# Kernel tuning notes

Measured on AMD Instinct MI355X. Metric: run time of the kernel, lower is better.

Reference implementation:

```python
import jax, jax.numpy as jnp
import numpy as np

N = 20000      # nodes
E = 120000     # directed edges (self-loops added in reference, per PyG default)
F_IN = 235
HID = 256
HEADS = 8
NEG_SLOPE = 0.2


def setup_inputs() -> dict:
    key = jax.random.key(0)
    ks = jax.random.split(key, 24)
    p = lambda k, shape: (jax.random.normal(k, shape, jnp.float32) * 0.05)
    inp = {}
    inp["x"] = jax.random.normal(ks[0], (N, F_IN), jnp.float32)
    inp["edge_index"] = jax.random.randint(ks[1], (2, E), 0, N, jnp.int32)
    # input projection
    inp["w_in"] = p(ks[2], (F_IN, HID)); inp["b_in"] = jnp.zeros((HID,), jnp.float32)
    # temporal MLP
    inp["w_t1"] = p(ks[3], (HID, HID)); inp["b_t1"] = jnp.zeros((HID,), jnp.float32)
    inp["w_t2"] = p(ks[4], (HID, HID)); inp["b_t2"] = jnp.zeros((HID,), jnp.float32)
    # GAT layer 1: heads=8, out_per_head=32, concat -> 256
    C1 = HID // HEADS
    inp["w_g1"] = p(ks[5], (HID, HEADS * C1)); inp["a_src1"] = p(ks[6], (HEADS, C1))
    inp["a_dst1"] = p(ks[7], (HEADS, C1)); inp["b_g1"] = jnp.zeros((HEADS * C1,), jnp.float32)
    # GAT layer 2: same shape
    inp["w_g2"] = p(ks[8], (HID, HEADS * C1)); inp["a_src2"] = p(ks[9], (HEADS, C1))
    inp["a_dst2"] = p(ks[10], (HEADS, C1)); inp["b_g2"] = jnp.zeros((HEADS * C1,), jnp.float32)
    # GAT layer 3: heads=8, out_per_head=256, concat -> 2048
    inp["w_g3"] = p(ks[11], (HID, HEADS * HID)); inp["a_src3"] = p(ks[12], (HEADS, HID))
    inp["a_dst3"] = p(ks[13], (HEADS, HID)); inp["b_g3"] = jnp.zeros((HEADS * HID,), jnp.float32)
    # classifier
    inp["w_c1"] = p(ks[14], (2 * HID, HID)); inp["b_c1"] = jnp.zeros((HID,), jnp.float32)
    inp["w_c2"] = p(ks[15], (HID, 2)); inp["b_c2"] = jnp.zeros((2,), jnp.float32)
    return inp


def _gat(x, src, dst, W, a_src, a_dst, b, C):
    """PyG-style GATConv: gather -> per-edge logits -> segment softmax -> scatter-add."""
    h = (x @ W).reshape(-1, HEADS, C)                       # [N, H, C]
    alpha_s = jnp.sum(h * a_src, axis=-1)                   # [N, H]
    alpha_d = jnp.sum(h * a_dst, axis=-1)                   # [N, H]
    e = jax.nn.leaky_relu(alpha_s[src] + alpha_d[dst], NEG_SLOPE)   # [Etot, H]
    m = jax.ops.segment_max(e, dst, num_segments=N)         # [N, H] (self-loops ensure non-empty)
    ex = jnp.exp(e - m[dst])
    den = jax.ops.segment_sum(ex, dst, num_segments=N)
    alpha = ex / (den[dst] + 1e-16)                          # [Etot, H]
    out = jax.ops.segment_sum(alpha[:, :, None] * h[src], dst, num_segments=N)  # [N, H, C]
    return out.reshape(-1, HEADS * C) + b


def reference(x, edge_index, w_in, b_in, w_t1, b_t1, w_t2, b_t2,
              w_g1, a_src1, a_dst1, b_g1, w_g2, a_src2, a_dst2, b_g2,
              w_g3, a_src3, a_dst3, b_g3, w_c1, b_c1, w_c2, b_c2):
    h = jax.nn.elu(x @ w_in + b_in)                          # [N, 256]
    t = jax.nn.relu(h @ w_t1 + b_t1) @ w_t2 + b_t2          # [N, 256] (dropout inactive in eval)
    loop = jnp.arange(N, dtype=edge_index.dtype)
    src = jnp.concatenate([edge_index[0], loop])
    dst = jnp.concatenate([edge_index[1], loop])
    g = jax.nn.elu(_gat(h, src, dst, w_g1, a_src1, a_dst1, b_g1, HID // HEADS))
    g = jax.nn.elu(_gat(g, src, dst, w_g2, a_src2, a_dst2, b_g2, HID // HEADS))
    g = jax.nn.elu(_gat(g, src, dst, w_g3, a_src3, a_dst3, b_g3, HID))  # [N, 2048]
    g = g.reshape(N, HEADS, HID).mean(axis=1)                # [N, 256]
    comb = jnp.concatenate([g, t], axis=-1)                  # [N, 512]
    logits = jax.nn.relu(comb @ w_c1 + b_c1) @ w_c2 + b_c2   # [N, 2]
    return logits
```

## Files before the change

kernel.cpp:

```cpp
#include <hip/hip_runtime.h>
#include <hip/hip_bf16.h>
#include <math.h>


#define HID 256
#define HEADS 8
#define FIN 235

typedef __attribute__((ext_vector_type(8))) short short8;
typedef __attribute__((ext_vector_type(4))) float floatx4;

__device__ __forceinline__ float elu_f(float x) { return x > 0.f ? x : __expf(x) - 1.f; }
__device__ __forceinline__ float bf2f(unsigned short u) {
  return __uint_as_float(((unsigned int)u) << 16);
}
__device__ __forceinline__ unsigned short f2bfu(float f) {
  union { __hip_bfloat16 b; unsigned short u; } c;
  c.b = __float2bfloat16(f);
  return c.u;
}

__global__ void xc_k(const float* __restrict__ x, __hip_bfloat16* __restrict__ xb,
                     const int* __restrict__ ei, int* __restrict__ deg,
                     const float* __restrict__ b2, float* __restrict__ out,
                     int M, int E, int xblocks, int cblocks) {
  int b = blockIdx.x;
  if (b < xblocks) {
    int id = b * 256 + threadIdx.x;
    if (id >= M * 256) return;
    int m = id >> 8, k = id & 255;
    xb[id] = (k < FIN) ? __float2bfloat16(x[(size_t)m * FIN + k]) : __float2bfloat16(0.f);
  } else if (b < xblocks + cblocks) {
    int i = (b - xblocks) * 256 + threadIdx.x;
    if (i < E) atomicAdd(&deg[ei[E + i]], 1);
  } else {
    int i = (b - xblocks - cblocks) * 256 + threadIdx.x;
    if (i < M * 2) out[i] = b2[i & 1];
  }
}

__global__ void wprep_k(const float* __restrict__ w_in, const float* __restrict__ w_t1,
                        const float* __restrict__ w_g1, const float* __restrict__ w_t2,
                        const float* __restrict__ w_g2, const float* __restrict__ w_c1,
                        const float* __restrict__ w_g3, const float* __restrict__ a_s3,
                        const float* __restrict__ a_d3, __hip_bfloat16* __restrict__ wtin,
                        __hip_bfloat16* __restrict__ wtpair, __hip_bfloat16* __restrict__ wtt2,
                        __hip_bfloat16* __restrict__ wtg2, __hip_bfloat16* __restrict__ wtc1,
                        __hip_bfloat16* __restrict__ wtg3s, float* __restrict__ apj) {
  __shared__ float t[32][33];
  int z = blockIdx.z;
  if (z == 14) {
    int idx = (blockIdx.y * 8 + blockIdx.x) * 256 + threadIdx.y * 32 + threadIdx.x;
    if (idx < 256 * 16) {
      int k = idx >> 4, o = idx & 15;
      int h = o >> 1;
      const float* av = (o & 1) ? (a_d3 + h * 256) : (a_s3 + h * 256);
      const float* wr = w_g3 + (size_t)k * 2048 + h * 256;
      float s = 0.f;
      for (int c = 0; c < 256; c++) s += wr[c] * av[c];
      apj[idx] = s;
    }
    return;
  }
  const float* src;
  __hip_bfloat16* dst;
  int K, Kpad, Nstride;
  if (z == 5) {
    src = w_c1; dst = wtc1; K = 512; Kpad = 512; Nstride = 256;
  } else {
    if (blockIdx.y >= 8) return;
    switch (z) {
      case 0: src = w_in; dst = wtin; K = FIN; Kpad = 256; Nstride = 256; break;
      case 1: src = w_t1; dst = wtpair; K = 256; Kpad = 256; Nstride = 256; break;
      case 2: src = w_g1; dst = wtpair + 256 * 256; K = 256; Kpad = 256; Nstride = 256; break;
      case 3: src = w_t2; dst = wtt2; K = 256; Kpad = 256; Nstride = 256; break;
      case 4: src = w_g2; dst = wtg2; K = 256; Kpad = 256; Nstride = 256; break;
      default: {
        int h = z - 6;
        src = w_g3 + h * 256; dst = wtg3s + h * 256; K = 256; Kpad = 2048; Nstride = 2048;
      }
    }
  }
  int nb = blockIdx.x * 32, kb = blockIdx.y * 32;
  int tx = threadIdx.x, ty = threadIdx.y;
#pragma unroll
  for (int j = 0; j < 32; j += 8) {
    int k = kb + ty + j;
    t[ty + j][tx] = (k < K) ? src[(size_t)k * Nstride + nb + tx] : 0.f;
  }
  __syncthreads();
#pragma unroll
  for (int j = 0; j < 32; j += 8) {
    int n = nb + ty + j;
    int k = kb + tx;
    dst[(size_t)n * Kpad + k] = __float2bfloat16(t[tx][ty + j]);
  }
}

__global__ void scan_k(const int* __restrict__ deg, int* __restrict__ rp, int n) {
  __shared__ int wsum[16];
  __shared__ int s_carry;
  int tid = threadIdx.x, lane = tid & 63, wid = tid >> 6;
  if (tid == 0) { s_carry = 0; rp[0] = 0; }
  __syncthreads();
  for (int base = 0; base < n; base += 1024) {
    int i = base + tid;
    int x = (i < n) ? (deg[i] + 1) : 0;
#pragma unroll
    for (int off = 1; off < 64; off <<= 1) {
      int y = __shfl_up(x, off);
      if (lane >= off) x += y;
    }
    if (lane == 63) wsum[wid] = x;
    __syncthreads();
    if (wid == 0 && lane < 16) {
      int s = wsum[lane];
#pragma unroll
      for (int off = 1; off < 16; off <<= 1) {
        int y = __shfl_up(s, off);
        if (lane >= off) s += y;
      }
      wsum[lane] = s;
    }
    __syncthreads();
    int offset = s_carry + (wid > 0 ? wsum[wid - 1] : 0);
    if (i < n) rp[i + 1] = offset + x;
    __syncthreads();
    if (tid == 1023) s_carry += wsum[15];
    __syncthreads();
  }
}

__global__ void fill_k(const int* __restrict__ ei, const int* __restrict__ rp,
                       int* __restrict__ fillc, int* __restrict__ colA, int E, int n) {
  int i = blockIdx.x * blockDim.x + threadIdx.x;
  if (i < E) {
    int d = ei[E + i];
    int pos = rp[d] + atomicAdd(&fillc[d], 1);
    colA[pos] = ei[i];
  } else if (i < E + n) {
    int v = i - E;
    int pos = rp[v] + atomicAdd(&fillc[v], 1);
    colA[pos] = v;
  }
}

template <int ACT, int ALPHA>
__global__ __launch_bounds__(256) void mgemm64_k(
    const __hip_bfloat16* __restrict__ A, const __hip_bfloat16* __restrict__ Bt,
    const float* __restrict__ bias, __hip_bfloat16* __restrict__ Cb,
    int ldc, int M, int N, int K, const float* __restrict__ a_s,
    const float* __restrict__ a_d, float* __restrict__ as_, float* __restrict__ ad_) {
  __shared__ short As[64 * 40];
  __shared__ short Bs[64 * 40];
  int tid = threadIdx.x;
  int row0 = blockIdx.y * 64, col0 = blockIdx.x * 64;
  int w = tid >> 6, lane = tid & 63;
  int wr = w >> 1, wc = w & 1;
  int quad = lane >> 4, l16 = lane & 15;
  floatx4 zero = {0.f, 0.f, 0.f, 0.f};
  floatx4 acc[2][2];
#pragma unroll
  for (int i = 0; i < 2; i++)
#pragma unroll
    for (int j = 0; j < 2; j++) acc[i][j] = zero;

  int srow = tid >> 2, sq = tid & 3;
  const __hip_bfloat16* Ap = A + (size_t)(row0 + srow) * K + sq * 8;
  const __hip_bfloat16* Bp = Bt + (size_t)(col0 + srow) * K + sq * 8;
  bool aok = (row0 + srow) < M;

  uint4 a1 = make_uint4(0, 0, 0, 0);
  if (aok) a1 = *(const uint4*)(Ap);
  uint4 b1 = *(const uint4*)(Bp);

  for (int k0 = 0; k0 < K; k0 += 32) {
    __syncthreads();
    *(uint4*)&As[srow * 40 + sq * 8] = a1;
    *(uint4*)&Bs[srow * 40 + sq * 8] = b1;
    int kn = k0 + 32;
    if (kn < K) {
      if (aok) a1 = *(const uint4*)(Ap + kn);
      b1 = *(const uint4*)(Bp + kn);
    }
    __syncthreads();
    short8 fa[2], fb[2];
#pragma unroll
    for (int i = 0; i < 2; i++) {
      fa[i] = *(const short8*)&As[(wr * 32 + i * 16 + l16) * 40 + quad * 8];
      fb[i] = *(const short8*)&Bs[(wc * 32 + i * 16 + l16) * 40 + quad * 8];
    }
#pragma unroll
    for (int mi = 0; mi < 2; mi++)
#pragma unroll
      for (int ni = 0; ni < 2; ni++)
        acc[mi][ni] = __builtin_amdgcn_mfma_f32_16x16x32_bf16(fa[mi], fb[ni], acc[mi][ni], 0, 0, 0);
  }

#pragma unroll
  for (int mi = 0; mi < 2; mi++) {
    int rbase = row0 + wr * 32 + mi * 16 + quad * 4;
#pragma unroll
    for (int ni = 0; ni < 2; ni++) {
      int c = col0 + wc * 32 + ni * 16 + l16;
      float bv = bias ? bias[c] : 0.f;
#pragma unroll
      for (int reg = 0; reg < 4; reg++) {
        int rr = rbase + reg;
        if (rr >= M) continue;
        float v = acc[mi][ni][reg] + bv;
        if (ACT == 1) v = fmaxf(v, 0.f);
        if (ACT == 2) v = elu_f(v);
        Cb[(size_t)rr * ldc + c] = __float2bfloat16(v);
      }
    }
  }

  if (ALPHA) {
    int h = 2 * blockIdx.x + wc;
    float aS0 = a_s[h * 32 + l16], aS1 = a_s[h * 32 + 16 + l16];
    float aD0 = a_d[h * 32 + l16], aD1 = a_d[h * 32 + 16 + l16];
#pragma unroll
    for (int mi = 0; mi < 2; mi++)
#pragma unroll
      for (int reg = 0; reg < 4; reg++) {
        float pS = acc[mi][0][reg] * aS0 + acc[mi][1][reg] * aS1;
        float pD = acc[mi][0][reg] * aD0 + acc[mi][1][reg] * aD1;
#pragma unroll
        for (int off = 1; off < 16; off <<= 1) {
          pS += __shfl_xor(pS, off);
          pD += __shfl_xor(pD, off);
        }
        if (l16 == 0) {
          int r = row0 + wr * 32 + mi * 16 + quad * 4 + reg;
          if (r < M) {
            as_[r * 8 + h] = pS;
            ad_[r * 8 + h] = pD;
          }
        }
      }
  }
}

__global__ __launch_bounds__(256) void mgemm_dual_k(
    const __hip_bfloat16* __restrict__ A, const __hip_bfloat16* __restrict__ Bt,
    const float* __restrict__ bias1, __hip_bfloat16* __restrict__ O1,
    __hip_bfloat16* __restrict__ O2, int M, const float* __restrict__ a_s1,
    const float* __restrict__ a_d1, float* __restrict__ as_, float* __restrict__ ad_) {
  const int K = 256;
  __shared__ short As[64 * 40];
  __shared__ short Bs[128 * 40];
  int tid = threadIdx.x;
  int row0 = blockIdx.y * 64, col0 = blockIdx.x * 128;
  int w = tid >> 6, lane = tid & 63;
  int wr = w >> 1, wc = w & 1;
  int quad = lane >> 4, l16 = lane & 15;
  floatx4 zero = {0.f, 0.f, 0.f, 0.f};
  floatx4 acc[2][4];
#pragma unroll
  for (int i = 0; i < 2; i++)
#pragma unroll
    for (int j = 0; j < 4; j++) acc[i][j] = zero;

  int srow = tid >> 2, sq = tid & 3;
  const __hip_bfloat16* Ap = A + (size_t)(row0 + srow) * K + sq * 8;
  const __hip_bfloat16* Bp1 = Bt + (size_t)(col0 + srow) * K + sq * 8;
  const __hip_bfloat16* Bp2 = Bt + (size_t)(col0 + 64 + srow) * K + sq * 8;
  bool aok = (row0 + srow) < M;

  uint4 a1 = make_uint4(0, 0, 0, 0);
  if (aok) a1 = *(const uint4*)(Ap);
  uint4 b1 = *(const uint4*)(Bp1);
  uint4 b2 = *(const uint4*)(Bp2);

  for (int k0 = 0; k0 < K; k0 += 32) {
    __syncthreads();
    *(uint4*)&As[srow * 40 + sq * 8] = a1;
    *(uint4*)&Bs[srow * 40 + sq * 8] = b1;
    *(uint4*)&Bs[(64 + srow) * 40 + sq * 8] = b2;
    int kn = k0 + 32;
    if (kn < K) {
      if (aok) a1 = *(const uint4*)(Ap + kn);
      b1 = *(const uint4*)(Bp1 + kn);
      b2 = *(const uint4*)(Bp2 + kn);
    }
    __syncthreads();
    short8 fa[2], fb[4];
#pragma unroll
    for (int i = 0; i < 2; i++)
      fa[i] = *(const short8*)&As[(wr * 32 + i * 16 + l16) * 40 + quad * 8];
#pragma unroll
    for (int i = 0; i < 4; i++)
      fb[i] = *(const short8*)&Bs[(wc * 64 + i * 16 + l16) * 40 + quad * 8];
#pragma unroll
    for (int mi = 0; mi < 2; mi++)
#pragma unroll
      for (int ni = 0; ni < 4; ni++)
        acc[mi][ni] = __builtin_amdgcn_mfma_f32_16x16x32_bf16(fa[mi], fb[ni], acc[mi][ni], 0, 0, 0);
  }

#pragma unroll
  for (int mi = 0; mi < 2; mi++) {
    int rbase = row0 + wr * 32 + mi * 16 + quad * 4;
#pragma unroll
    for (int ni = 0; ni < 4; ni++) {
      int c = col0 + wc * 64 + ni * 16 + l16;
      bool first = c < 256;
      float bv = first ? bias1[c] : 0.f;
      int cc = first ? c : (c - 256);
#pragma unroll
      for (int reg = 0; reg < 4; reg++) {
        int rr = rbase + reg;
        if (rr >= M) continue;
        float v = acc[mi][ni][reg] + bv;
        if (first) v = fmaxf(v, 0.f);
        __hip_bfloat16* dst = first ? O1 : O2;
        dst[(size_t)rr * 256 + cc] = __float2bfloat16(v);
      }
    }
  }

  if (blockIdx.x >= 2) {
    int hb = (blockIdx.x - 2) * 4 + wc * 2;
    float aSA0 = a_s1[hb * 32 + l16], aSA1 = a_s1[hb * 32 + 16 + l16];
    float aDA0 = a_d1[hb * 32 + l16], aDA1 = a_d1[hb * 32 + 16 + l16];
    float aSB0 = a_s1[(hb + 1) * 32 + l16], aSB1 = a_s1[(hb + 1) * 32 + 16 + l16];
    float aDB0 = a_d1[(hb + 1) * 32 + l16], aDB1 = a_d1[(hb + 1) * 32 + 16 + l16];
#pragma unroll
    for (int mi = 0; mi < 2; mi++)
#pragma unroll
      for (int reg = 0; reg < 4; reg++) {
        float pSA = acc[mi][0][reg] * aSA0 + acc[mi][1][reg] * aSA1;
        float pDA = acc[mi][0][reg] * aDA0 + acc[mi][1][reg] * aDA1;
        float pSB = acc[mi][2][reg] * aSB0 + acc[mi][3][reg] * aSB1;
        float pDB = acc[mi][2][reg] * aDB0 + acc[mi][3][reg] * aDB1;
#pragma unroll
        for (int off = 1; off < 16; off <<= 1) {
          pSA += __shfl_xor(pSA, off);
          pDA += __shfl_xor(pDA, off);
          pSB += __shfl_xor(pSB, off);
          pDB += __shfl_xor(pDB, off);
        }
        if (l16 == 0) {
          int r = row0 + wr * 32 + mi * 16 + quad * 4 + reg;
          if (r < M) {
            as_[r * 8 + hb] = pSA;
            ad_[r * 8 + hb] = pDA;
            as_[r * 8 + hb + 1] = pSB;
            ad_[r * 8 + hb + 1] = pDB;
          }
        }
      }
  }
}

__global__ __launch_bounds__(256) void mgemm3_k(
    const __hip_bfloat16* __restrict__ A, const __hip_bfloat16* __restrict__ Bt,
    const float* __restrict__ bias, __hip_bfloat16* __restrict__ comb, int M) {
  const int K = 2048;
  __shared__ short As[64 * 40];
  __shared__ short Bs[64 * 40];
  int tid = threadIdx.x;
  int mg = (M + 63) >> 6;
  int total = mg * 4;
  int F = blockIdx.y * 4 + blockIdx.x;
  int Fmain = (total >> 5) << 5;
  int bx, by;
  if (F < Fmain) {
    by = (F >> 5) * 8 + (F & 7);
    bx = (F >> 3) & 3;
  } else {
    by = ((total >> 5) << 3) + ((F - Fmain) >> 2);
    bx = (F - Fmain) & 3;
  }
  int row0 = by * 64, col0 = bx * 64;
  int w = tid >> 6, lane = tid & 63;
  int wr = w >> 1, wc = w & 1;
  int quad = lane >> 4, l16 = lane & 15;
  floatx4 zero = {0.f, 0.f, 0.f, 0.f};
  floatx4 acc[2][2], sum[2][2];
#pragma unroll
  for (int i = 0; i < 2; i++)
#pragma unroll
    for (int j = 0; j < 2; j++) { acc[i][j] = zero; sum[i][j] = zero; }

  int srow = tid >> 2, sq = tid & 3;
  const __hip_bfloat16* Ap = A + (size_t)(row0 + srow) * K + sq * 8;
  const __hip_bfloat16* Bp = Bt + (size_t)(col0 + srow) * K + sq * 8;
  bool aok = (row0 + srow) < M;

  uint4 a1 = make_uint4(0, 0, 0, 0);
  if (aok) a1 = *(const uint4*)(Ap);
  uint4 b1 = *(const uint4*)(Bp);

  for (int k0 = 0; k0 < K; k0 += 32) {
    __syncthreads();
    *(uint4*)&As[srow * 40 + sq * 8] = a1;
    *(uint4*)&Bs[srow * 40 + sq * 8] = b1;
    int kn = k0 + 32;
    if (kn < K) {
      if (aok) a1 = *(const uint4*)(Ap + kn);
      b1 = *(const uint4*)(Bp + kn);
    }
    __syncthreads();
    short8 fa[2], fb[2];
#pragma unroll
    for (int i = 0; i < 2; i++) {
      fa[i] = *(const short8*)&As[(wr * 32 + i * 16 + l16) * 40 + quad * 8];
      fb[i] = *(const short8*)&Bs[(wc * 32 + i * 16 + l16) * 40 + quad * 8];
    }
#pragma unroll
    for (int mi = 0; mi < 2; mi++)
#pragma unroll
      for (int ni = 0; ni < 2; ni++)
        acc[mi][ni] = __builtin_amdgcn_mfma_f32_16x16x32_bf16(fa[mi], fb[ni], acc[mi][ni], 0, 0, 0);
    if (((k0 + 32) & 255) == 0) {
      int h = k0 >> 8;
#pragma unroll
      for (int mi = 0; mi < 2; mi++)
#pragma unroll
        for (int ni = 0; ni < 2; ni++) {
          int c = col0 + wc * 32 + ni * 16 + l16;
          float bv = bias[h * 256 + c];
#pragma unroll
          for (int reg = 0; reg < 4; reg++) {
            sum[mi][ni][reg] += elu_f(acc[mi][ni][reg] + bv);
            acc[mi][ni][reg] = 0.f;
          }
        }
    }
  }

#pragma unroll
  for (int mi = 0; mi < 2; mi++) {
    int rbase = row0 + wr * 32 + mi * 16 + quad * 4;
#pragma unroll
    for (int ni = 0; ni < 2; ni++) {
      int c = col0 + wc * 32 + ni * 16 + l16;
#pragma unroll
      for (int reg = 0; reg < 4; reg++) {
        int rr = rbase + reg;
        if (rr >= M) continue;
        comb[(size_t)rr * 512 + c] = __float2bfloat16(sum[mi][ni][reg] * 0.125f);
      }
    }
  }
}

__global__ __launch_bounds__(256) void mgemm_cls_k(
    const __hip_bfloat16* __restrict__ A, const __hip_bfloat16* __restrict__ Bt,
    const float* __restrict__ bias, const float* __restrict__ w2,
    float* __restrict__ out, int M) {
  const int K = 512;
  __shared__ short As[64 * 40];
  __shared__ short Bs[128 * 40];
  __shared__ float ls[64][2][2];
  int tid = threadIdx.x;
  int row0 = blockIdx.y * 64, col0 = blockIdx.x * 128;
  int w = tid >> 6, lane = tid & 63;
  int wr = w >> 1, wc = w & 1;
  int quad = lane >> 4, l16 = lane & 15;
  floatx4 zero = {0.f, 0.f, 0.f, 0.f};
  floatx4 acc[2][4];
#pragma unroll
  for (int i = 0; i < 2; i++)
#pragma unroll
    for (int j = 0; j < 4; j++) acc[i][j] = zero;

  int srow = tid >> 2, sq = tid & 3;
  const __hip_bfloat16* Ap = A + (size_t)(row0 + srow) * K + sq * 8;
  const __hip_bfloat16* Bp1 = Bt + (size_t)(col0 + srow) * K + sq * 8;
  const __hip_bfloat16* Bp2 = Bt + (size_t)(col0 + 64 + srow) * K + sq * 8;
  bool aok = (row0 + srow) < M;

  uint4 a1 = make_uint4(0, 0, 0, 0);
  if (aok) a1 = *(const uint4*)(Ap);
  uint4 b1 = *(const uint4*)(Bp1);
  uint4 b2 = *(const uint4*)(Bp2);

  for (int k0 = 0; k0 < K; k0 += 32) {
    __syncthreads();
    *(uint4*)&As[srow * 40 + sq * 8] = a1;
    *(uint4*)&Bs[srow * 40 + sq * 8] = b1;
    *(uint4*)&Bs[(64 + srow) * 40 + sq * 8] = b2;
    int kn = k0 + 32;
    if (kn < K) {
      if (aok) a1 = *(const uint4*)(Ap + kn);
      b1 = *(const uint4*)(Bp1 + kn);
      b2 = *(const uint4*)(Bp2 + kn);
    }
    __syncthreads();
    short8 fa[2], fb[4];
#pragma unroll
    for (int i = 0; i < 2; i++)
      fa[i] = *(const short8*)&As[(wr * 32 + i * 16 + l16) * 40 + quad * 8];
#pragma unroll
    for (int i = 0; i < 4; i++)
      fb[i] = *(const short8*)&Bs[(wc * 64 + i * 16 + l16) * 40 + quad * 8];
#pragma unroll
    for (int mi = 0; mi < 2; mi++)
#pragma unroll
      for (int ni = 0; ni < 4; ni++)
        acc[mi][ni] = __builtin_amdgcn_mfma_f32_16x16x32_bf16(fa[mi], fb[ni], acc[mi][ni], 0, 0, 0);
  }

  float p0[2][4], p1[2][4];
#pragma unroll
  for (int mi = 0; mi < 2; mi++)
#pragma unroll
    for (int reg = 0; reg < 4; reg++) { p0[mi][reg] = 0.f; p1[mi][reg] = 0.f; }
#pragma unroll
  for (int mi = 0; mi < 2; mi++)
#pragma unroll
    for (int ni = 0; ni < 4; ni++) {
      int c = col0 + wc * 64 + ni * 16 + l16;
      float bv = bias[c];
      float w20 = w2[c * 2 + 0], w21 = w2[c * 2 + 1];
#pragma unroll
      for (int reg = 0; reg < 4; reg++) {
        float v = fmaxf(acc[mi][ni][reg] + bv, 0.f);
        p0[mi][reg] += v * w20;
        p1[mi][reg] += v * w21;
      }
    }
#pragma unroll
  for (int off = 1; off < 16; off <<= 1)
#pragma unroll
    for (int mi = 0; mi < 2; mi++)
#pragma unroll
      for (int reg = 0; reg < 4; reg++) {
        p0[mi][reg] += __shfl_xor(p0[mi][reg], off);
        p1[mi][reg] += __shfl_xor(p1[mi][reg], off);
      }
  if (l16 == 0) {
#pragma unroll
    for (int mi = 0; mi < 2; mi++)
#pragma unroll
      for (int reg = 0; reg < 4; reg++) {
        int rl = wr * 32 + mi * 16 + quad * 4 + reg;
        ls[rl][wc][0] = p0[mi][reg];
        ls[rl][wc][1] = p1[mi][reg];
      }
  }
  __syncthreads();
  if (tid < 64) {
    int r = row0 + tid;
    if (r < M) {
      atomicAdd(&out[r * 2 + 0], ls[tid][0][0] + ls[tid][1][0]);
      atomicAdd(&out[r * 2 + 1], ls[tid][0][1] + ls[tid][1][1]);
    }
  }
}

__global__ __launch_bounds__(256) void alpha3_k(const __hip_bfloat16* __restrict__ g2,
                                                const float* __restrict__ apj,
                                                float* __restrict__ as_, float* __restrict__ ad_,
                                                int M) {
  __shared__ float sapj[4096];
  int tid = threadIdx.x;
  for (int i = tid; i < 4096; i += 256) sapj[i] = apj[i];
  __syncthreads();
  int nl = tid >> 4, o = tid & 15;
  int n = blockIdx.x * 16 + nl;
  if (n >= M) return;
  const __hip_bfloat16* row = g2 + (size_t)n * 256;
  float s = 0.f;
  for (int cc = 0; cc < 256; cc += 8) {
    short8 v8 = *(const short8*)(row + cc);
#pragma unroll
    for (int j = 0; j < 8; j++)
      s += bf2f((unsigned short)v8[j]) * sapj[(cc + j) * 16 + o];
  }
  if (o & 1) ad_[n * 8 + (o >> 1)] = s;
  else as_[n * 8 + (o >> 1)] = s;
}

__global__ __launch_bounds__(256) void aggf_k(const int* __restrict__ rp,
                                              const int* __restrict__ col,
                                              const __hip_bfloat16* __restrict__ hW,
                                              const float* __restrict__ as_,
                                              const float* __restrict__ ad_,
                                              const float* __restrict__ bias,
                                              __hip_bfloat16* __restrict__ out, int M) {
  int dst = blockIdx.x * 4 + (threadIdx.x >> 6);
  if (dst >= M) return;
  int t = threadIdx.x & 63;
  int h = t >> 3, c = t << 2;
  int beg = rp[dst], end = rp[dst + 1];
  float adv = ad_[dst * 8 + h];
  float m = -3.4e38f, den = 0.f;
  float a0 = 0.f, a1 = 0.f, a2 = 0.f, a3 = 0.f;
  int i = beg;
  for (; i + 4 <= end; i += 4) {
    int s0 = col[i], s1 = col[i + 1], s2 = col[i + 2], s3 = col[i + 3];
    float e0 = as_[s0 * 8 + h] + adv;
    float e1 = as_[s1 * 8 + h] + adv;
    float e2 = as_[s2 * 8 + h] + adv;
    float e3 = as_[s3 * 8 + h] + adv;
    union { uint2 u; unsigned short us[4]; } v0, v1, v2, v3;
    v0.u = *(const uint2*)(hW + (size_t)s0 * HID + c);
    v1.u = *(const uint2*)(hW + (size_t)s1 * HID + c);
    v2.u = *(const uint2*)(hW + (size_t)s2 * HID + c);
    v3.u = *(const uint2*)(hW + (size_t)s3 * HID + c);
    e0 = e0 > 0.f ? e0 : 0.2f * e0;
    e1 = e1 > 0.f ? e1 : 0.2f * e1;
    e2 = e2 > 0.f ? e2 : 0.2f * e2;
    e3 = e3 > 0.f ? e3 : 0.2f * e3;
    float mb = fmaxf(fmaxf(e0, e1), fmaxf(e2, e3));
    float mn = fmaxf(m, mb);
    float sc = __expf(m - mn);
    float w0 = __expf(e0 - mn), w1 = __expf(e1 - mn);
    float w2 = __expf(e2 - mn), w3 = __expf(e3 - mn);
    m = mn;
    den = den * sc + (w0 + w1 + w2 + w3);
    a0 = a0 * sc + w0 * bf2f(v0.us[0]) + w1 * bf2f(v1.us[0]) + w2 * bf2f(v2.us[0]) + w3 * bf2f(v3.us[0]);
    a1 = a1 * sc + w0 * bf2f(v0.us[1]) + w1 * bf2f(v1.us[1]) + w2 * bf2f(v2.us[1]) + w3 * bf2f(v3.us[1]);
    a2 = a2 * sc + w0 * bf2f(v0.us[2]) + w1 * bf2f(v1.us[2]) + w2 * bf2f(v2.us[2]) + w3 * bf2f(v3.us[2]);
    a3 = a3 * sc + w0 * bf2f(v0.us[3]) + w1 * bf2f(v1.us[3]) + w2 * bf2f(v2.us[3]) + w3 * bf2f(v3.us[3]);
  }
  for (; i < end; i++) {
    int s = col[i];
    float e = as_[s * 8 + h] + adv;
    e = e > 0.f ? e : 0.2f * e;
    float mn = fmaxf(m, e);
    float sc = __expf(m - mn);
    float wgt = __expf(e - mn);
    m = mn;
    union { uint2 u; unsigned short us[4]; } uu;
    uu.u = *(const uint2*)(hW + (size_t)s * HID + c);
    den = den * sc + wgt;
    a0 = a0 * sc + wgt * bf2f(uu.us[0]);
    a1 = a1 * sc + wgt * bf2f(uu.us[1]);
    a2 = a2 * sc + wgt * bf2f(uu.us[2]);
    a3 = a3 * sc + wgt * bf2f(uu.us[3]);
  }
  float inv = 1.f / (den + 1e-16f);
  out[(size_t)dst * HID + c + 0] = __float2bfloat16(elu_f(a0 * inv + bias[c + 0]));
  out[(size_t)dst * HID + c + 1] = __float2bfloat16(elu_f(a1 * inv + bias[c + 1]));
  out[(size_t)dst * HID + c + 2] = __float2bfloat16(elu_f(a2 * inv + bias[c + 2]));
  out[(size_t)dst * HID + c + 3] = __float2bfloat16(elu_f(a3 * inv + bias[c + 3]));
}

__global__ __launch_bounds__(256) void esoft_k(const int* __restrict__ rp,
                                               const int* __restrict__ col,
                                               const float* __restrict__ as_,
                                               const float* __restrict__ ad_,
                                               float* __restrict__ ex,
                                               float* __restrict__ invden, int M) {
  int dst = blockIdx.x * 4 + (threadIdx.x >> 6);
  if (dst >= M) return;
  int lane = threadIdx.x & 63;
  int es = lane >> 3, h = lane & 7;
  int beg = rp[dst], end = rp[dst + 1];
  float adv = ad_[dst * 8 + h];
  float m = -3.4e38f;
  for (int i = beg + es; i < end; i += 8) {
    float e = as_[col[i] * 8 + h] + adv;
    e = e > 0.f ? e : 0.2f * e;
    m = fmaxf(m, e);
  }
  m = fmaxf(m, __shfl_xor(m, 8));
  m = fmaxf(m, __shfl_xor(m, 16));
  m = fmaxf(m, __shfl_xor(m, 32));
  float den = 0.f;
  for (int i = beg + es; i < end; i += 8) {
    float e = as_[col[i] * 8 + h] + adv;
    e = e > 0.f ? e : 0.2f * e;
    float v = __expf(e - m);
    ex[(size_t)i * 8 + h] = v;
    den += v;
  }
  den += __shfl_xor(den, 8);
  den += __shfl_xor(den, 16);
  den += __shfl_xor(den, 32);
  if (es == 0) invden[dst * 8 + h] = 1.f / (den + 1e-16f);
}

__global__ __launch_bounds__(256) void agg3_k(const int* __restrict__ rp,
                                              const int* __restrict__ col,
                                              const __hip_bfloat16* __restrict__ g2,
                                              const float* __restrict__ ex,
                                              const float* __restrict__ invden,
                                              __hip_bfloat16* __restrict__ outA, int M) {
  int dst = blockIdx.x * 4 + (threadIdx.x >> 6);
  if (dst >= M) return;
  int t = threadIdx.x & 63;
  int beg = rp[dst], end = rp[dst + 1];
  float acc[4][8];
#pragma unroll
  for (int ch = 0; ch < 4; ch++)
#pragma unroll
    for (int h = 0; h < 8; h++) acc[ch][h] = 0.f;
  int i = beg;
  for (; i + 2 <= end; i += 2) {
    int s0 = col[i], s1 = col[i + 1];
    union { uint2 u; unsigned short us[4]; } u0, u1;
    u0.u = *(const uint2*)(g2 + (size_t)s0 * 256 + t * 4);
    u1.u = *(const uint2*)(g2 + (size_t)s1 * 256 + t * 4);
    float4 wa0 = *(const float4*)(ex + (size_t)i * 8);
    float4 wa1 = *(const float4*)(ex + (size_t)i * 8 + 4);
    float4 wb0 = *(const float4*)(ex + (size_t)(i + 1) * 8);
    float4 wb1 = *(const float4*)(ex + (size_t)(i + 1) * 8 + 4);
#pragma unroll
    for (int ch = 0; ch < 4; ch++) {
      float va = bf2f(u0.us[ch]), vb = bf2f(u1.us[ch]);
      acc[ch][0] += wa0.x * va + wb0.x * vb;
      acc[ch][1] += wa0.y * va + wb0.y * vb;
      acc[ch][2] += wa0.z * va + wb0.z * vb;
      acc[ch][3] += wa0.w * va + wb0.w * vb;
      acc[ch][4] += wa1.x * va + wb1.x * vb;
      acc[ch][5] += wa1.y * va + wb1.y * vb;
      acc[ch][6] += wa1.z * va + wb1.z * vb;
      acc[ch][7] += wa1.w * va + wb1.w * vb;
    }
  }
  for (; i < end; i++) {
    int s = col[i];
    float4 w0 = *(const float4*)(ex + (size_t)i * 8);
    float4 w1 = *(const float4*)(ex + (size_t)i * 8 + 4);
    union { uint2 u; unsigned short us[4]; } uu;
    uu.u = *(const uint2*)(g2 + (size_t)s * 256 + t * 4);
#pragma unroll
    for (int ch = 0; ch < 4; ch++) {
      float v = bf2f(uu.us[ch]);
      acc[ch][0] += w0.x * v; acc[ch][1] += w0.y * v;
      acc[ch][2] += w0.z * v; acc[ch][3] += w0.w * v;
      acc[ch][4] += w1.x * v; acc[ch][5] += w1.y * v;
      acc[ch][6] += w1.z * v; acc[ch][7] += w1.w * v;
    }
  }
#pragma unroll
  for (int h = 0; h < 8; h++) {
    float inv = invden[dst * 8 + h];
    union { uint2 u; unsigned short us[4]; } pk;
#pragma unroll
    for (int ch = 0; ch < 4; ch++) pk.us[ch] = f2bfu(acc[ch][h] * inv);
    *(uint2*)(outA + (size_t)dst * 2048 + h * 256 + t * 4) = pk.u;
  }
}

extern "C" void kernel_launch(void* const* d_in, const int* in_sizes, int n_in,
                              void* d_out, int out_size, void* d_ws, size_t ws_size,
                              hipStream_t stream) {
  const float* x      = (const float*)d_in[0];
  const int*   ei     = (const int*)d_in[1];
  const float* w_in   = (const float*)d_in[2];
  const float* b_in   = (const float*)d_in[3];
  const float* w_t1   = (const float*)d_in[4];
  const float* b_t1   = (const float*)d_in[5];
  const float* w_t2   = (const float*)d_in[6];
  const float* b_t2   = (const float*)d_in[7];
  const float* w_g1   = (const float*)d_in[8];
  const float* a_src1 = (const float*)d_in[9];
  const float* a_dst1 = (const float*)d_in[10];
  const float* b_g1   = (const float*)d_in[11];
  const float* w_g2   = (const float*)d_in[12];
  const float* a_src2 = (const float*)d_in[13];
  const float* a_dst2 = (const float*)d_in[14];
  const float* b_g2   = (const float*)d_in[15];
  const float* w_g3   = (const float*)d_in[16];
  const float* a_src3 = (const float*)d_in[17];
  const float* a_dst3 = (const float*)d_in[18];
  const float* b_g3   = (const float*)d_in[19];
  const float* w_c1   = (const float*)d_in[20];
  const float* b_c1   = (const float*)d_in[21];
  const float* w_c2   = (const float*)d_in[22];
  const float* b_c2   = (const float*)d_in[23];
  const int M = in_sizes[0] / FIN;
  const int E = in_sizes[1] / 2;
  (void)n_in; (void)out_size; (void)ws_size;

  char* wsb = (char*)d_ws;
  size_t off = 0;
  auto alloc = [&](size_t bytes) {
    void* p = wsb + off;
    off = (off + bytes + 255) & ~(size_t)255;
    return p;
  };
  typedef __hip_bfloat16 bf;
  bf* xb     = (bf*)alloc((size_t)M * 256 * 2);
  bf* wtin   = (bf*)alloc(256 * 256 * 2);
  bf* wtpair = (bf*)alloc(512 * 256 * 2);
  bf* wtt2   = (bf*)alloc(256 * 256 * 2);
  bf* wtg2   = (bf*)alloc(256 * 256 * 2);
  bf* wtg3s  = (bf*)alloc(256 * 2048 * 2);
  bf* wtc1   = (bf*)alloc(256 * 512 * 2);
  bf* actA   = (bf*)alloc((size_t)M * HID * 2);
  bf* actB   = (bf*)alloc((size_t)M * HID * 2);
  bf* hW1    = (bf*)alloc((size_t)M * HID * 2);
  bf* comb   = (bf*)alloc((size_t)M * 2 * HID * 2);
  bf* hWb    = (bf*)alloc((size_t)M * 2048 * 2);
  float* as_ = (float*)alloc((size_t)M * 8 * 4);
  float* ad_ = (float*)alloc((size_t)M * 8 * 4);
  float* apj = (float*)alloc(256 * 16 * 4);
  float* exw = (float*)alloc((size_t)(E + M) * 8 * 4);
  float* ivd = (float*)alloc((size_t)M * 8 * 4);
  int* degfill = (int*)alloc((size_t)2 * M * 4);
  int* deg   = degfill;
  int* fillc = degfill + M;
  int* rp    = (int*)alloc((size_t)(M + 1) * 4);
  int* colA  = (int*)alloc((size_t)(E + M) * 4);

  hipMemsetAsync(degfill, 0, (size_t)2 * M * 4, stream);
  int xblocks = (M * 256 + 255) / 256;
  int cblocks = (E + 255) / 256;
  int oblocks = (M * 2 + 255) / 256;
  xc_k<<<xblocks + cblocks + oblocks, 256, 0, stream>>>(x, xb, ei, deg, b_c2, (float*)d_out,
                                                        M, E, xblocks, cblocks);
  wprep_k<<<dim3(8, 16, 15), dim3(32, 8), 0, stream>>>(
      w_in, w_t1, w_g1, w_t2, w_g2, w_c1, w_g3, a_src3, a_dst3,
      wtin, wtpair, wtt2, wtg2, wtc1, wtg3s, apj);

  scan_k<<<1, 1024, 0, stream>>>(deg, rp, M);
  fill_k<<<(E + M + 255) / 256, 256, 0, stream>>>(ei, rp, fillc, colA, E, M);

  int eg = (M + 3) / 4;
  int mg = (M + 63) / 64;

  mgemm64_k<2, 0><<<dim3(4, mg), 256, 0, stream>>>(xb, wtin, b_in, actA, HID, M, HID, 256,
                                                   nullptr, nullptr, nullptr, nullptr);
  mgemm_dual_k<<<dim3(4, mg), 256, 0, stream>>>(actA, wtpair, b_t1, actB, hW1, M,
                                                a_src1, a_dst1, as_, ad_);
  mgemm64_k<0, 0><<<dim3(4, mg), 256, 0, stream>>>(actB, wtt2, b_t2, comb + HID, 2 * HID,
                                                   M, HID, 256, nullptr, nullptr, nullptr, nullptr);

  aggf_k<<<eg, 256, 0, stream>>>(rp, colA, hW1, as_, ad_, b_g1, actB, M);

  mgemm64_k<0, 1><<<dim3(4, mg), 256, 0, stream>>>(actB, wtg2, nullptr, hW1, HID, M, HID, 256,
                                                   a_src2, a_dst2, as_, ad_);
  aggf_k<<<eg, 256, 0, stream>>>(rp, colA, hW1, as_, ad_, b_g2, actA, M);

  alpha3_k<<<(M + 15) / 16, 256, 0, stream>>>(actA, apj, as_, ad_, M);
  esoft_k<<<eg, 256, 0, stream>>>(rp, colA, as_, ad_, exw, ivd, M);
  agg3_k<<<eg, 256, 0, stream>>>(rp, colA, actA, exw, ivd, hWb, M);
  mgemm3_k<<<dim3(4, mg), 256, 0, stream>>>(hWb, wtg3s, b_g3, comb, M);

  mgemm_cls_k<<<dim3(2, mg), 256, 0, stream>>>(comb, wtc1, b_c1, w_c2, (float*)d_out, M);
}
```

Before: 377.9 us.

## Merge independent kernels into combined launches and unroll layer-3 aggregation by four

The CSR fill pass is merged into the input-projection GEMM launch, and the temporal second GEMM is merged with the first GAT aggregation, with the block index deciding which role each block plays. The GAT1 output now goes to a separate scratch region inside hWb, so the aggregation no longer overwrites actB while the GEMM still reads it. The layer-3 aggregation loop is unrolled from 2 to 4 edges to put more gathers in flight. The goal is fewer launches and better GPU fill from running independent work together, at the cost of mixed-role blocks sharing one register and LDS budget.

```diff
diff --git a/kernel.cpp b/kernel.cpp
--- a/kernel.cpp
+++ b/kernel.cpp
@@ -131,30 +131,15 @@
   }
 }
 
-__global__ void fill_k(const int* __restrict__ ei, const int* __restrict__ rp,
-                       int* __restrict__ fillc, int* __restrict__ colA, int E, int n) {
-  int i = blockIdx.x * blockDim.x + threadIdx.x;
-  if (i < E) {
-    int d = ei[E + i];
-    int pos = rp[d] + atomicAdd(&fillc[d], 1);
-    colA[pos] = ei[i];
-  } else if (i < E + n) {
-    int v = i - E;
-    int pos = rp[v] + atomicAdd(&fillc[v], 1);
-    colA[pos] = v;
-  }
-}
-
 template <int ACT, int ALPHA>
-__global__ __launch_bounds__(256) void mgemm64_k(
-    const __hip_bfloat16* __restrict__ A, const __hip_bfloat16* __restrict__ Bt,
-    const float* __restrict__ bias, __hip_bfloat16* __restrict__ Cb,
-    int ldc, int M, int N, int K, const float* __restrict__ a_s,
-    const float* __restrict__ a_d, float* __restrict__ as_, float* __restrict__ ad_) {
-  __shared__ short As[64 * 40];
-  __shared__ short Bs[64 * 40];
+__device__ __forceinline__ void gemm64_body(
+    short* As, short* Bs, const __hip_bfloat16* __restrict__ A,
+    const __hip_bfloat16* __restrict__ Bt, const float* __restrict__ bias,
+    __hip_bfloat16* __restrict__ Cb, int ldc, int M, int K, int bx, int by,
+    const float* __restrict__ a_s, const float* __restrict__ a_d,
+    float* __restrict__ as_, float* __restrict__ ad_) {
   int tid = threadIdx.x;
-  int row0 = blockIdx.y * 64, col0 = blockIdx.x * 64;
+  int row0 = by * 64, col0 = bx * 64;
   int w = tid >> 6, lane = tid & 63;
   int wr = w >> 1, wc = w & 1;
   int quad = lane >> 4, l16 = lane & 15;
@@ -217,7 +202,7 @@
   }
 
   if (ALPHA) {
-    int h = 2 * blockIdx.x + wc;
+    int h = 2 * bx + wc;
     float aS0 = a_s[h * 32 + l16], aS1 = a_s[h * 32 + 16 + l16];
     float aD0 = a_d[h * 32 + l16], aD1 = a_d[h * 32 + 16 + l16];
 #pragma unroll
@@ -242,347 +227,12 @@
   }
 }
 
-__global__ __launch_bounds__(256) void mgemm_dual_k(
-    const __hip_bfloat16* __restrict__ A, const __hip_bfloat16* __restrict__ Bt,
-    const float* __restrict__ bias1, __hip_bfloat16* __restrict__ O1,
-    __hip_bfloat16* __restrict__ O2, int M, const float* __restrict__ a_s1,
-    const float* __restrict__ a_d1, float* __restrict__ as_, float* __restrict__ ad_) {
-  const int K = 256;
-  __shared__ short As[64 * 40];
-  __shared__ short Bs[128 * 40];
-  int tid = threadIdx.x;
-  int row0 = blockIdx.y * 64, col0 = blockIdx.x * 128;
-  int w = tid >> 6, lane = tid & 63;
-  int wr = w >> 1, wc = w & 1;
-  int quad = lane >> 4, l16 = lane & 15;
-  floatx4 zero = {0.f, 0.f, 0.f, 0.f};
-  floatx4 acc[2][4];
-#pragma unroll
-  for (int i = 0; i < 2; i++)
-#pragma unroll
-    for (int j = 0; j < 4; j++) acc[i][j] = zero;
-
-  int srow = tid >> 2, sq = tid & 3;
-  const __hip_bfloat16* Ap = A + (size_t)(row0 + srow) * K + sq * 8;
-  const __hip_bfloat16* Bp1 = Bt + (size_t)(col0 + srow) * K + sq * 8;
-  const __hip_bfloat16* Bp2 = Bt + (size_t)(col0 + 64 + srow) * K + sq * 8;
-  bool aok = (row0 + srow) < M;
-
-  uint4 a1 = make_uint4(0, 0, 0, 0);
-  if (aok) a1 = *(const uint4*)(Ap);
-  uint4 b1 = *(const uint4*)(Bp1);
-  uint4 b2 = *(const uint4*)(Bp2);
-
-  for (int k0 = 0; k0 < K; k0 += 32) {
-    __syncthreads();
-    *(uint4*)&As[srow * 40 + sq * 8] = a1;
-    *(uint4*)&Bs[srow * 40 + sq * 8] = b1;
-    *(uint4*)&Bs[(64 + srow) * 40 + sq * 8] = b2;
-    int kn = k0 + 32;
-    if (kn < K) {
-      if (aok) a1 = *(const uint4*)(Ap + kn);
-      b1 = *(const uint4*)(Bp1 + kn);
-      b2 = *(const uint4*)(Bp2 + kn);
-    }
-    __syncthreads();
-    short8 fa[2], fb[4];
-#pragma unroll
-    for (int i = 0; i < 2; i++)
-      fa[i] = *(const short8*)&As[(wr * 32 + i * 16 + l16) * 40 + quad * 8];
-#pragma unroll
-    for (int i = 0; i < 4; i++)
-      fb[i] = *(const short8*)&Bs[(wc * 64 + i * 16 + l16) * 40 + quad * 8];
-#pragma unroll
-    for (int mi = 0; mi < 2; mi++)
-#pragma unroll
-      for (int ni = 0; ni < 4; ni++)
-        acc[mi][ni] = __builtin_amdgcn_mfma_f32_16x16x32_bf16(fa[mi], fb[ni], acc[mi][ni], 0, 0, 0);
-  }
-
-#pragma unroll
-  for (int mi = 0; mi < 2; mi++) {
-    int rbase = row0 + wr * 32 + mi * 16 + quad * 4;
-#pragma unroll
-    for (int ni = 0; ni < 4; ni++) {
-      int c = col0 + wc * 64 + ni * 16 + l16;
-      bool first = c < 256;
-      float bv = first ? bias1[c] : 0.f;
-      int cc = first ? c : (c - 256);
-#pragma unroll
-      for (int reg = 0; reg < 4; reg++) {
-        int rr = rbase + reg;
-        if (rr >= M) continue;
-        float v = acc[mi][ni][reg] + bv;
-        if (first) v = fmaxf(v, 0.f);
-        __hip_bfloat16* dst = first ? O1 : O2;
-        dst[(size_t)rr * 256 + cc] = __float2bfloat16(v);
-      }
-    }
-  }
-
-  if (blockIdx.x >= 2) {
-    int hb = (blockIdx.x - 2) * 4 + wc * 2;
-    float aSA0 = a_s1[hb * 32 + l16], aSA1 = a_s1[hb * 32 + 16 + l16];
-    float aDA0 = a_d1[hb * 32 + l16], aDA1 = a_d1[hb * 32 + 16 + l16];
-    float aSB0 = a_s1[(hb + 1) * 32 + l16], aSB1 = a_s1[(hb + 1) * 32 + 16 + l16];
-    float aDB0 = a_d1[(hb + 1) * 32 + l16], aDB1 = a_d1[(hb + 1) * 32 + 16 + l16];
-#pragma unroll
-    for (int mi = 0; mi < 2; mi++)
-#pragma unroll
-      for (int reg = 0; reg < 4; reg++) {
-        float pSA = acc[mi][0][reg] * aSA0 + acc[mi][1][reg] * aSA1;
-        float pDA = acc[mi][0][reg] * aDA0 + acc[mi][1][reg] * aDA1;
-        float pSB = acc[mi][2][reg] * aSB0 + acc[mi][3][reg] * aSB1;
-        float pDB = acc[mi][2][reg] * aDB0 + acc[mi][3][reg] * aDB1;
-#pragma unroll
-        for (int off = 1; off < 16; off <<= 1) {
-          pSA += __shfl_xor(pSA, off);
-          pDA += __shfl_xor(pDA, off);
-          pSB += __shfl_xor(pSB, off);
-          pDB += __shfl_xor(pDB, off);
-        }
-        if (l16 == 0) {
-          int r = row0 + wr * 32 + mi * 16 + quad * 4 + reg;
-          if (r < M) {
-            as_[r * 8 + hb] = pSA;
-            ad_[r * 8 + hb] = pDA;
-            as_[r * 8 + hb + 1] = pSB;
-            ad_[r * 8 + hb + 1] = pDB;
-          }
-        }
-      }
-  }
-}
-
-__global__ __launch_bounds__(256) void mgemm3_k(
-    const __hip_bfloat16* __restrict__ A, const __hip_bfloat16* __restrict__ Bt,
-    const float* __restrict__ bias, __hip_bfloat16* __restrict__ comb, int M) {
-  const int K = 2048;
-  __shared__ short As[64 * 40];
-  __shared__ short Bs[64 * 40];
-  int tid = threadIdx.x;
-  int mg = (M + 63) >> 6;
-  int total = mg * 4;
-  int F = blockIdx.y * 4 + blockIdx.x;
-  int Fmain = (total >> 5) << 5;
-  int bx, by;
-  if (F < Fmain) {
-    by = (F >> 5) * 8 + (F & 7);
-    bx = (F >> 3) & 3;
-  } else {
-    by = ((total >> 5) << 3) + ((F - Fmain) >> 2);
-    bx = (F - Fmain) & 3;
-  }
-  int row0 = by * 64, col0 = bx * 64;
-  int w = tid >> 6, lane = tid & 63;
-  int wr = w >> 1, wc = w & 1;
-  int quad = lane >> 4, l16 = lane & 15;
-  floatx4 zero = {0.f, 0.f, 0.f, 0.f};
-  floatx4 acc[2][2], sum[2][2];
-#pragma unroll
-  for (int i = 0; i < 2; i++)
-#pragma unroll
-    for (int j = 0; j < 2; j++) { acc[i][j] = zero; sum[i][j] = zero; }
-
-  int srow = tid >> 2, sq = tid & 3;
-  const __hip_bfloat16* Ap = A + (size_t)(row0 + srow) * K + sq * 8;
-  const __hip_bfloat16* Bp = Bt + (size_t)(col0 + srow) * K + sq * 8;
-  bool aok = (row0 + srow) < M;
-
-  uint4 a1 = make_uint4(0, 0, 0, 0);
-  if (aok) a1 = *(const uint4*)(Ap);
-  uint4 b1 = *(const uint4*)(Bp);
-
-  for (int k0 = 0; k0 < K; k0 += 32) {
-    __syncthreads();
-    *(uint4*)&As[srow * 40 + sq * 8] = a1;
-    *(uint4*)&Bs[srow * 40 + sq * 8] = b1;
-    int kn = k0 + 32;
-    if (kn < K) {
-      if (aok) a1 = *(const uint4*)(Ap + kn);
-      b1 = *(const uint4*)(Bp + kn);
-    }
-    __syncthreads();
-    short8 fa[2], fb[2];
-#pragma unroll
-    for (int i = 0; i < 2; i++) {
-      fa[i] = *(const short8*)&As[(wr * 32 + i * 16 + l16) * 40 + quad * 8];
-      fb[i] = *(const short8*)&Bs[(wc * 32 + i * 16 + l16) * 40 + quad * 8];
-    }
-#pragma unroll
-    for (int mi = 0; mi < 2; mi++)
-#pragma unroll
-      for (int ni = 0; ni < 2; ni++)
-        acc[mi][ni] = __builtin_amdgcn_mfma_f32_16x16x32_bf16(fa[mi], fb[ni], acc[mi][ni], 0, 0, 0);
-    if (((k0 + 32) & 255) == 0) {
-      int h = k0 >> 8;
-#pragma unroll
-      for (int mi = 0; mi < 2; mi++)
-#pragma unroll
-        for (int ni = 0; ni < 2; ni++) {
-          int c = col0 + wc * 32 + ni * 16 + l16;
-          float bv = bias[h * 256 + c];
-#pragma unroll
-          for (int reg = 0; reg < 4; reg++) {
-            sum[mi][ni][reg] += elu_f(acc[mi][ni][reg] + bv);
-            acc[mi][ni][reg] = 0.f;
-          }
-        }
-    }
-  }
-
-#pragma unroll
-  for (int mi = 0; mi < 2; mi++) {
-    int rbase = row0 + wr * 32 + mi * 16 + quad * 4;
-#pragma unroll
-    for (int ni = 0; ni < 2; ni++) {
-      int c = col0 + wc * 32 + ni * 16 + l16;
-#pragma unroll
-      for (int reg = 0; reg < 4; reg++) {
-        int rr = rbase + reg;
-        if (rr >= M) continue;
-        comb[(size_t)rr * 512 + c] = __float2bfloat16(sum[mi][ni][reg] * 0.125f);
-      }
-    }
-  }
-}
-
-__global__ __launch_bounds__(256) void mgemm_cls_k(
-    const __hip_bfloat16* __restrict__ A, const __hip_bfloat16* __restrict__ Bt,
-    const float* __restrict__ bias, const float* __restrict__ w2,
-    float* __restrict__ out, int M) {
-  const int K = 512;
-  __shared__ short As[64 * 40];
-  __shared__ short Bs[128 * 40];
-  __shared__ float ls[64][2][2];
-  int tid = threadIdx.x;
-  int row0 = blockIdx.y * 64, col0 = blockIdx.x * 128;
-  int w = tid >> 6, lane = tid & 63;
-  int wr = w >> 1, wc = w & 1;
-  int quad = lane >> 4, l16 = lane & 15;
-  floatx4 zero = {0.f, 0.f, 0.f, 0.f};
-  floatx4 acc[2][4];
-#pragma unroll
-  for (int i = 0; i < 2; i++)
-#pragma unroll
-    for (int j = 0; j < 4; j++) acc[i][j] = zero;
-
-  int srow = tid >> 2, sq = tid & 3;
-  const __hip_bfloat16* Ap = A + (size_t)(row0 + srow) * K + sq * 8;
-  const __hip_bfloat16* Bp1 = Bt + (size_t)(col0 + srow) * K + sq * 8;
-  const __hip_bfloat16* Bp2 = Bt + (size_t)(col0 + 64 + srow) * K + sq * 8;
-  bool aok = (row0 + srow) < M;
-
-  uint4 a1 = make_uint4(0, 0, 0, 0);
-  if (aok) a1 = *(const uint4*)(Ap);
-  uint4 b1 = *(const uint4*)(Bp1);
-  uint4 b2 = *(const uint4*)(Bp2);
-
-  for (int k0 = 0; k0 < K; k0 += 32) {
-    __syncthreads();
-    *(uint4*)&As[srow * 40 + sq * 8] = a1;
-    *(uint4*)&Bs[srow * 40 + sq * 8] = b1;
-    *(uint4*)&Bs[(64 + srow) * 40 + sq * 8] = b2;
-    int kn = k0 + 32;
-    if (kn < K) {
-      if (aok) a1 = *(const uint4*)(Ap + kn);
-      b1 = *(const uint4*)(Bp1 + kn);
-      b2 = *(const uint4*)(Bp2 + kn);
-    }
-    __syncthreads();
-    short8 fa[2], fb[4];
-#pragma unroll
-    for (int i = 0; i < 2; i++)
-      fa[i] = *(const short8*)&As[(wr * 32 + i * 16 + l16) * 40 + quad * 8];
-#pragma unroll
-    for (int i = 0; i < 4; i++)
-      fb[i] = *(const short8*)&Bs[(wc * 64 + i * 16 + l16) * 40 + quad * 8];
-#pragma unroll
-    for (int mi = 0; mi < 2; mi++)
-#pragma unroll
-      for (int ni = 0; ni < 4; ni++)
-        acc[mi][ni] = __builtin_amdgcn_mfma_f32_16x16x32_bf16(fa[mi], fb[ni], acc[mi][ni], 0, 0, 0);
-  }
-
-  float p0[2][4], p1[2][4];
-#pragma unroll
-  for (int mi = 0; mi < 2; mi++)
-#pragma unroll
-    for (int reg = 0; reg < 4; reg++) { p0[mi][reg] = 0.f; p1[mi][reg] = 0.f; }
-#pragma unroll
-  for (int mi = 0; mi < 2; mi++)
-#pragma unroll
-    for (int ni = 0; ni < 4; ni++) {
-      int c = col0 + wc * 64 + ni * 16 + l16;
-      float bv = bias[c];
-      float w20 = w2[c * 2 + 0], w21 = w2[c * 2 + 1];
-#pragma unroll
-      for (int reg = 0; reg < 4; reg++) {
-        float v = fmaxf(acc[mi][ni][reg] + bv, 0.f);
-        p0[mi][reg] += v * w20;
-        p1[mi][reg] += v * w21;
-      }
-    }
-#pragma unroll
-  for (int off = 1; off < 16; off <<= 1)
-#pragma unroll
-    for (int mi = 0; mi < 2; mi++)
-#pragma unroll
-      for (int reg = 0; reg < 4; reg++) {
-        p0[mi][reg] += __shfl_xor(p0[mi][reg], off);
-        p1[mi][reg] += __shfl_xor(p1[mi][reg], off);
-      }
-  if (l16 == 0) {
-#pragma unroll
-    for (int mi = 0; mi < 2; mi++)
-#pragma unroll
-      for (int reg = 0; reg < 4; reg++) {
-        int rl = wr * 32 + mi * 16 + quad * 4 + reg;
-        ls[rl][wc][0] = p0[mi][reg];
-        ls[rl][wc][1] = p1[mi][reg];
-      }
-  }
-  __syncthreads();
-  if (tid < 64) {
-    int r = row0 + tid;
-    if (r < M) {
-      atomicAdd(&out[r * 2 + 0], ls[tid][0][0] + ls[tid][1][0]);
-      atomicAdd(&out[r * 2 + 1], ls[tid][0][1] + ls[tid][1][1]);
-    }
-  }
-}
-
-__global__ __launch_bounds__(256) void alpha3_k(const __hip_bfloat16* __restrict__ g2,
-                                                const float* __restrict__ apj,
-                                                float* __restrict__ as_, float* __restrict__ ad_,
-                                                int M) {
-  __shared__ float sapj[4096];
-  int tid = threadIdx.x;
-  for (int i = tid; i < 4096; i += 256) sapj[i] = apj[i];
-  __syncthreads();
-  int nl = tid >> 4, o = tid & 15;
-  int n = blockIdx.x * 16 + nl;
-  if (n >= M) return;
-  const __hip_bfloat16* row = g2 + (size_t)n * 256;
-  float s = 0.f;
-  for (int cc = 0; cc < 256; cc += 8) {
-    short8 v8 = *(const short8*)(row + cc);
-#pragma unroll
-    for (int j = 0; j < 8; j++)
-      s += bf2f((unsigned short)v8[j]) * sapj[(cc + j) * 16 + o];
-  }
-  if (o & 1) ad_[n * 8 + (o >> 1)] = s;
-  else as_[n * 8 + (o >> 1)] = s;
-}
-
-__global__ __launch_bounds__(256) void aggf_k(const int* __restrict__ rp,
-                                              const int* __restrict__ col,
-                                              const __hip_bfloat16* __restrict__ hW,
-                                              const float* __restrict__ as_,
-                                              const float* __restrict__ ad_,
-                                              const float* __restrict__ bias,
-                                              __hip_bfloat16* __restrict__ out, int M) {
-  int dst = blockIdx.x * 4 + (threadIdx.x >> 6);
+__device__ __forceinline__ void aggf_body(
+    const int* __restrict__ rp, const int* __restrict__ col,
+    const __hip_bfloat16* __restrict__ hW, const float* __restrict__ as_,
+    const float* __restrict__ ad_, const float* __restrict__ bias,
+    __hip_bfloat16* __restrict__ out, int M, int blk) {
+  int dst = blk * 4 + (threadIdx.x >> 6);
   if (dst >= M) return;
   int t = threadIdx.x & 63;
   int h = t >> 3, c = t << 2;
@@ -641,6 +291,404 @@
   out[(size_t)dst * HID + c + 3] = __float2bfloat16(elu_f(a3 * inv + bias[c + 3]));
 }
 
+__global__ __launch_bounds__(256) void fusedA_k(
+    const __hip_bfloat16* __restrict__ xb, const __hip_bfloat16* __restrict__ wtin,
+    const float* __restrict__ b_in, __hip_bfloat16* __restrict__ actA,
+    const int* __restrict__ ei, const int* __restrict__ rp, int* __restrict__ fillc,
+    int* __restrict__ colA, int M, int E, int gemmBlocks) {
+  __shared__ short As[64 * 40];
+  __shared__ short Bs[64 * 40];
+  int b = blockIdx.x;
+  if (b < gemmBlocks) {
+    gemm64_body<2, 0>(As, Bs, xb, wtin, b_in, actA, HID, M, 256, b & 3, b >> 2,
+                      nullptr, nullptr, nullptr, nullptr);
+  } else {
+    int i = (b - gemmBlocks) * 256 + threadIdx.x;
+    if (i < E) {
+      int d = ei[E + i];
+      int pos = rp[d] + atomicAdd(&fillc[d], 1);
+      colA[pos] = ei[i];
+    } else if (i < E + M) {
+      int v = i - E;
+      int pos = rp[v] + atomicAdd(&fillc[v], 1);
+      colA[pos] = v;
+    }
+  }
+}
+
+__global__ __launch_bounds__(256) void fusedB_k(
+    const __hip_bfloat16* __restrict__ actB, const __hip_bfloat16* __restrict__ wtt2,
+    const float* __restrict__ b_t2, __hip_bfloat16* __restrict__ combT,
+    const int* __restrict__ rp, const int* __restrict__ col,
+    const __hip_bfloat16* __restrict__ hW1, const float* __restrict__ as_,
+    const float* __restrict__ ad_, const float* __restrict__ b_g1,
+    __hip_bfloat16* __restrict__ g1, int M, int gemmBlocks) {
+  __shared__ short As[64 * 40];
+  __shared__ short Bs[64 * 40];
+  int b = blockIdx.x;
+  if (b < gemmBlocks) {
+    gemm64_body<0, 0>(As, Bs, actB, wtt2, b_t2, combT, 2 * HID, M, 256, b & 3, b >> 2,
+                      nullptr, nullptr, nullptr, nullptr);
+  } else {
+    aggf_body(rp, col, hW1, as_, ad_, b_g1, g1, M, b - gemmBlocks);
+  }
+}
+
+template <int ACT, int ALPHA>
+__global__ __launch_bounds__(256) void mgemm64_k(
+    const __hip_bfloat16* __restrict__ A, const __hip_bfloat16* __restrict__ Bt,
+    const float* __restrict__ bias, __hip_bfloat16* __restrict__ Cb,
+    int ldc, int M, int N, int K, const float* __restrict__ a_s,
+    const float* __restrict__ a_d, float* __restrict__ as_, float* __restrict__ ad_) {
+  __shared__ short As[64 * 40];
+  __shared__ short Bs[64 * 40];
+  gemm64_body<ACT, ALPHA>(As, Bs, A, Bt, bias, Cb, ldc, M, K, blockIdx.x, blockIdx.y,
+                          a_s, a_d, as_, ad_);
+}
+
+__global__ __launch_bounds__(256) void aggf_k(const int* __restrict__ rp,
+                                              const int* __restrict__ col,
+                                              const __hip_bfloat16* __restrict__ hW,
+                                              const float* __restrict__ as_,
+                                              const float* __restrict__ ad_,
+                                              const float* __restrict__ bias,
+                                              __hip_bfloat16* __restrict__ out, int M) {
+  aggf_body(rp, col, hW, as_, ad_, bias, out, M, blockIdx.x);
+}
+
+__global__ __launch_bounds__(256) void mgemm_dual_k(
+    const __hip_bfloat16* __restrict__ A, const __hip_bfloat16* __restrict__ Bt,
+    const float* __restrict__ bias1, __hip_bfloat16* __restrict__ O1,
+    __hip_bfloat16* __restrict__ O2, int M, const float* __restrict__ a_s1,
+    const float* __restrict__ a_d1, float* __restrict__ as_, float* __restrict__ ad_) {
+  const int K = 256;
+  __shared__ short As[64 * 40];
+  __shared__ short Bs[128 * 40];
+  int tid = threadIdx.x;
+  int row0 = blockIdx.y * 64, col0 = blockIdx.x * 128;
+  int w = tid >> 6, lane = tid & 63;
+  int wr = w >> 1, wc = w & 1;
+  int quad = lane >> 4, l16 = lane & 15;
+  floatx4 zero = {0.f, 0.f, 0.f, 0.f};
+  floatx4 acc[2][4];
+#pragma unroll
+  for (int i = 0; i < 2; i++)
+#pragma unroll
+    for (int j = 0; j < 4; j++) acc[i][j] = zero;
+
+  int srow = tid >> 2, sq = tid & 3;
+  const __hip_bfloat16* Ap = A + (size_t)(row0 + srow) * K + sq * 8;
+  const __hip_bfloat16* Bp1 = Bt + (size_t)(col0 + srow) * K + sq * 8;
+  const __hip_bfloat16* Bp2 = Bt + (size_t)(col0 + 64 + srow) * K + sq * 8;
+  bool aok = (row0 + srow) < M;
+
+  uint4 a1 = make_uint4(0, 0, 0, 0);
+  if (aok) a1 = *(const uint4*)(Ap);
+  uint4 b1 = *(const uint4*)(Bp1);
+  uint4 b2 = *(const uint4*)(Bp2);
+
+  for (int k0 = 0; k0 < K; k0 += 32) {
+    __syncthreads();
+    *(uint4*)&As[srow * 40 + sq * 8] = a1;
+    *(uint4*)&Bs[srow * 40 + sq * 8] = b1;
+    *(uint4*)&Bs[(64 + srow) * 40 + sq * 8] = b2;
+    int kn = k0 + 32;
+    if (kn < K) {
+      if (aok) a1 = *(const uint4*)(Ap + kn);
+      b1 = *(const uint4*)(Bp1 + kn);
+      b2 = *(const uint4*)(Bp2 + kn);
+    }
+    __syncthreads();
+    short8 fa[2], fb[4];
+#pragma unroll
+    for (int i = 0; i < 2; i++)
+      fa[i] = *(const short8*)&As[(wr * 32 + i * 16 + l16) * 40 + quad * 8];
+#pragma unroll
+    for (int i = 0; i < 4; i++)
+      fb[i] = *(const short8*)&Bs[(wc * 64 + i * 16 + l16) * 40 + quad * 8];
+#pragma unroll
+    for (int mi = 0; mi < 2; mi++)
+#pragma unroll
+      for (int ni = 0; ni < 4; ni++)
+        acc[mi][ni] = __builtin_amdgcn_mfma_f32_16x16x32_bf16(fa[mi], fb[ni], acc[mi][ni], 0, 0, 0);
+  }
+
+#pragma unroll
+  for (int mi = 0; mi < 2; mi++) {
+    int rbase = row0 + wr * 32 + mi * 16 + quad * 4;
+#pragma unroll
+    for (int ni = 0; ni < 4; ni++) {
+      int c = col0 + wc * 64 + ni * 16 + l16;
+      bool first = c < 256;
+      float bv = first ? bias1[c] : 0.f;
+      int cc = first ? c : (c - 256);
+#pragma unroll
+      for (int reg = 0; reg < 4; reg++) {
+        int rr = rbase + reg;
+        if (rr >= M) continue;
+        float v = acc[mi][ni][reg] + bv;
+        if (first) v = fmaxf(v, 0.f);
+        __hip_bfloat16* dst = first ? O1 : O2;
+        dst[(size_t)rr * 256 + cc] = __float2bfloat16(v);
+      }
+    }
+  }
+
+  if (blockIdx.x >= 2) {
+    int hb = (blockIdx.x - 2) * 4 + wc * 2;
+    float aSA0 = a_s1[hb * 32 + l16], aSA1 = a_s1[hb * 32 + 16 + l16];
+    float aDA0 = a_d1[hb * 32 + l16], aDA1 = a_d1[hb * 32 + 16 + l16];
+    float aSB0 = a_s1[(hb + 1) * 32 + l16], aSB1 = a_s1[(hb + 1) * 32 + 16 + l16];
+    float aDB0 = a_d1[(hb + 1) * 32 + l16], aDB1 = a_d1[(hb + 1) * 32 + 16 + l16];
+#pragma unroll
+    for (int mi = 0; mi < 2; mi++)
+#pragma unroll
+      for (int reg = 0; reg < 4; reg++) {
+        float pSA = acc[mi][0][reg] * aSA0 + acc[mi][1][reg] * aSA1;
+        float pDA = acc[mi][0][reg] * aDA0 + acc[mi][1][reg] * aDA1;
+        float pSB = acc[mi][2][reg] * aSB0 + acc[mi][3][reg] * aSB1;
+        float pDB = acc[mi][2][reg] * aDB0 + acc[mi][3][reg] * aDB1;
+#pragma unroll
+        for (int off = 1; off < 16; off <<= 1) {
+          pSA += __shfl_xor(pSA, off);
+          pDA += __shfl_xor(pDA, off);
+          pSB += __shfl_xor(pSB, off);
+          pDB += __shfl_xor(pDB, off);
+        }
+        if (l16 == 0) {
+          int r = row0 + wr * 32 + mi * 16 + quad * 4 + reg;
+          if (r < M) {
+            as_[r * 8 + hb] = pSA;
+            ad_[r * 8 + hb] = pDA;
+            as_[r * 8 + hb + 1] = pSB;
+            ad_[r * 8 + hb + 1] = pDB;
+          }
+        }
+      }
+  }
+}
+
+__global__ __launch_bounds__(256) void mgemm3_k(
+    const __hip_bfloat16* __restrict__ A, const __hip_bfloat16* __restrict__ Bt,
+    const float* __restrict__ bias, __hip_bfloat16* __restrict__ comb, int M) {
+  const int K = 2048;
+  __shared__ short As[64 * 40];
+  __shared__ short Bs[64 * 40];
+  int tid = threadIdx.x;
+  int mg = (M + 63) >> 6;
+  int total = mg * 4;
+  int F = blockIdx.y * 4 + blockIdx.x;
+  int Fmain = (total >> 5) << 5;
+  int bx, by;
+  if (F < Fmain) {
+    by = (F >> 5) * 8 + (F & 7);
+    bx = (F >> 3) & 3;
+  } else {
+    by = ((total >> 5) << 3) + ((F - Fmain) >> 2);
+    bx = (F - Fmain) & 3;
+  }
+  int row0 = by * 64, col0 = bx * 64;
+  int w = tid >> 6, lane = tid & 63;
+  int wr = w >> 1, wc = w & 1;
+  int quad = lane >> 4, l16 = lane & 15;
+  floatx4 zero = {0.f, 0.f, 0.f, 0.f};
+  floatx4 acc[2][2], sum[2][2];
+#pragma unroll
+  for (int i = 0; i < 2; i++)
+#pragma unroll
+    for (int j = 0; j < 2; j++) { acc[i][j] = zero; sum[i][j] = zero; }
+
+  int srow = tid >> 2, sq = tid & 3;
+  const __hip_bfloat16* Ap = A + (size_t)(row0 + srow) * K + sq * 8;
+  const __hip_bfloat16* Bp = Bt + (size_t)(col0 + srow) * K + sq * 8;
+  bool aok = (row0 + srow) < M;
+
+  uint4 a1 = make_uint4(0, 0, 0, 0);
+  if (aok) a1 = *(const uint4*)(Ap);
+  uint4 b1 = *(const uint4*)(Bp);
+
+  for (int k0 = 0; k0 < K; k0 += 32) {
+    __syncthreads();
+    *(uint4*)&As[srow * 40 + sq * 8] = a1;
+    *(uint4*)&Bs[srow * 40 + sq * 8] = b1;
+    int kn = k0 + 32;
+    if (kn < K) {
+      if (aok) a1 = *(const uint4*)(Ap + kn);
+      b1 = *(const uint4*)(Bp + kn);
+    }
+    __syncthreads();
+    short8 fa[2], fb[2];
+#pragma unroll
+    for (int i = 0; i < 2; i++) {
+      fa[i] = *(const short8*)&As[(wr * 32 + i * 16 + l16) * 40 + quad * 8];
+      fb[i] = *(const short8*)&Bs[(wc * 32 + i * 16 + l16) * 40 + quad * 8];
+    }
+#pragma unroll
+    for (int mi = 0; mi < 2; mi++)
+#pragma unroll
+      for (int ni = 0; ni < 2; ni++)
+        acc[mi][ni] = __builtin_amdgcn_mfma_f32_16x16x32_bf16(fa[mi], fb[ni], acc[mi][ni], 0, 0, 0);
+    if (((k0 + 32) & 255) == 0) {
+      int h = k0 >> 8;
+#pragma unroll
+      for (int mi = 0; mi < 2; mi++)
+#pragma unroll
+        for (int ni = 0; ni < 2; ni++) {
+          int c = col0 + wc * 32 + ni * 16 + l16;
+          float bv = bias[h * 256 + c];
+#pragma unroll
+          for (int reg = 0; reg < 4; reg++) {
+            sum[mi][ni][reg] += elu_f(acc[mi][ni][reg] + bv);
+            acc[mi][ni][reg] = 0.f;
+          }
+        }
+    }
+  }
+
+#pragma unroll
+  for (int mi = 0; mi < 2; mi++) {
+    int rbase = row0 + wr * 32 + mi * 16 + quad * 4;
+#pragma unroll
+    for (int ni = 0; ni < 2; ni++) {
+      int c = col0 + wc * 32 + ni * 16 + l16;
+#pragma unroll
+      for (int reg = 0; reg < 4; reg++) {
+        int rr = rbase + reg;
+        if (rr >= M) continue;
+        comb[(size_t)rr * 512 + c] = __float2bfloat16(sum[mi][ni][reg] * 0.125f);
+      }
+    }
+  }
+}
+
+__global__ __launch_bounds__(256) void mgemm_cls_k(
+    const __hip_bfloat16* __restrict__ A, const __hip_bfloat16* __restrict__ Bt,
+    const float* __restrict__ bias, const float* __restrict__ w2,
+    float* __restrict__ out, int M) {
+  const int K = 512;
+  __shared__ short As[64 * 40];
+  __shared__ short Bs[128 * 40];
+  __shared__ float ls[64][2][2];
+  int tid = threadIdx.x;
+  int row0 = blockIdx.y * 64, col0 = blockIdx.x * 128;
+  int w = tid >> 6, lane = tid & 63;
+  int wr = w >> 1, wc = w & 1;
+  int quad = lane >> 4, l16 = lane & 15;
+  floatx4 zero = {0.f, 0.f, 0.f, 0.f};
+  floatx4 acc[2][4];
+#pragma unroll
+  for (int i = 0; i < 2; i++)
+#pragma unroll
+    for (int j = 0; j < 4; j++) acc[i][j] = zero;
+
+  int srow = tid >> 2, sq = tid & 3;
+  const __hip_bfloat16* Ap = A + (size_t)(row0 + srow) * K + sq * 8;
+  const __hip_bfloat16* Bp1 = Bt + (size_t)(col0 + srow) * K + sq * 8;
+  const __hip_bfloat16* Bp2 = Bt + (size_t)(col0 + 64 + srow) * K + sq * 8;
+  bool aok = (row0 + srow) < M;
+
+  uint4 a1 = make_uint4(0, 0, 0, 0);
+  if (aok) a1 = *(const uint4*)(Ap);
+  uint4 b1 = *(const uint4*)(Bp1);
+  uint4 b2 = *(const uint4*)(Bp2);
+
+  for (int k0 = 0; k0 < K; k0 += 32) {
+    __syncthreads();
+    *(uint4*)&As[srow * 40 + sq * 8] = a1;
+    *(uint4*)&Bs[srow * 40 + sq * 8] = b1;
+    *(uint4*)&Bs[(64 + srow) * 40 + sq * 8] = b2;
+    int kn = k0 + 32;
+    if (kn < K) {
+      if (aok) a1 = *(const uint4*)(Ap + kn);
+      b1 = *(const uint4*)(Bp1 + kn);
+      b2 = *(const uint4*)(Bp2 + kn);
+    }
+    __syncthreads();
+    short8 fa[2], fb[4];
+#pragma unroll
+    for (int i = 0; i < 2; i++)
+      fa[i] = *(const short8*)&As[(wr * 32 + i * 16 + l16) * 40 + quad * 8];
+#pragma unroll
+    for (int i = 0; i < 4; i++)
+      fb[i] = *(const short8*)&Bs[(wc * 64 + i * 16 + l16) * 40 + quad * 8];
+#pragma unroll
+    for (int mi = 0; mi < 2; mi++)
+#pragma unroll
+      for (int ni = 0; ni < 4; ni++)
+        acc[mi][ni] = __builtin_amdgcn_mfma_f32_16x16x32_bf16(fa[mi], fb[ni], acc[mi][ni], 0, 0, 0);
+  }
+
+  float p0[2][4], p1[2][4];
+#pragma unroll
+  for (int mi = 0; mi < 2; mi++)
+#pragma unroll
+    for (int reg = 0; reg < 4; reg++) { p0[mi][reg] = 0.f; p1[mi][reg] = 0.f; }
+#pragma unroll
+  for (int mi = 0; mi < 2; mi++)
+#pragma unroll
+    for (int ni = 0; ni < 4; ni++) {
+      int c = col0 + wc * 64 + ni * 16 + l16;
+      float bv = bias[c];
+      float w20 = w2[c * 2 + 0], w21 = w2[c * 2 + 1];
+#pragma unroll
+      for (int reg = 0; reg < 4; reg++) {
+        float v = fmaxf(acc[mi][ni][reg] + bv, 0.f);
+        p0[mi][reg] += v * w20;
+        p1[mi][reg] += v * w21;
+      }
+    }
+#pragma unroll
+  for (int off = 1; off < 16; off <<= 1)
+#pragma unroll
+    for (int mi = 0; mi < 2; mi++)
+#pragma unroll
+      for (int reg = 0; reg < 4; reg++) {
+        p0[mi][reg] += __shfl_xor(p0[mi][reg], off);
+        p1[mi][reg] += __shfl_xor(p1[mi][reg], off);
+      }
+  if (l16 == 0) {
+#pragma unroll
+    for (int mi = 0; mi < 2; mi++)
+#pragma unroll
+      for (int reg = 0; reg < 4; reg++) {
+        int rl = wr * 32 + mi * 16 + quad * 4 + reg;
+        ls[rl][wc][0] = p0[mi][reg];
+        ls[rl][wc][1] = p1[mi][reg];
+      }
+  }
+  __syncthreads();
+  if (tid < 64) {
+    int r = row0 + tid;
+    if (r < M) {
+      atomicAdd(&out[r * 2 + 0], ls[tid][0][0] + ls[tid][1][0]);
+      atomicAdd(&out[r * 2 + 1], ls[tid][0][1] + ls[tid][1][1]);
+    }
+  }
+}
+
+__global__ __launch_bounds__(256) void alpha3_k(const __hip_bfloat16* __restrict__ g2,
+                                                const float* __restrict__ apj,
+                                                float* __restrict__ as_, float* __restrict__ ad_,
+                                                int M) {
+  __shared__ float sapj[4096];
+  int tid = threadIdx.x;
+  for (int i = tid; i < 4096; i += 256) sapj[i] = apj[i];
+  __syncthreads();
+  int nl = tid >> 4, o = tid & 15;
+  int n = blockIdx.x * 16 + nl;
+  if (n >= M) return;
+  const __hip_bfloat16* row = g2 + (size_t)n * 256;
+  float s = 0.f;
+  for (int cc = 0; cc < 256; cc += 8) {
+    short8 v8 = *(const short8*)(row + cc);
+#pragma unroll
+    for (int j = 0; j < 8; j++)
+      s += bf2f((unsigned short)v8[j]) * sapj[(cc + j) * 16 + o];
+  }
+  if (o & 1) ad_[n * 8 + (o >> 1)] = s;
+  else as_[n * 8 + (o >> 1)] = s;
+}
+
 __global__ __launch_bounds__(256) void esoft_k(const int* __restrict__ rp,
                                                const int* __restrict__ col,
                                                const float* __restrict__ as_,
@@ -692,26 +740,33 @@
 #pragma unroll
     for (int h = 0; h < 8; h++) acc[ch][h] = 0.f;
   int i = beg;
-  for (; i + 2 <= end; i += 2) {
-    int s0 = col[i], s1 = col[i + 1];
-    union { uint2 u; unsigned short us[4]; } u0, u1;
+  for (; i + 4 <= end; i += 4) {
+    int s0 = col[i], s1 = col[i + 1], s2 = col[i + 2], s3 = col[i + 3];
+    union { uint2 u; unsigned short us[4]; } u0, u1, u2, u3;
     u0.u = *(const uint2*)(g2 + (size_t)s0 * 256 + t * 4);
     u1.u = *(const uint2*)(g2 + (size_t)s1 * 256 + t * 4);
+    u2.u = *(const uint2*)(g2 + (size_t)s2 * 256 + t * 4);
+    u3.u = *(const uint2*)(g2 + (size_t)s3 * 256 + t * 4);
     float4 wa0 = *(const float4*)(ex + (size_t)i * 8);
     float4 wa1 = *(const float4*)(ex + (size_t)i * 8 + 4);
     float4 wb0 = *(const float4*)(ex + (size_t)(i + 1) * 8);
     float4 wb1 = *(const float4*)(ex + (size_t)(i + 1) * 8 + 4);
+    float4 wc0 = *(const float4*)(ex + (size_t)(i + 2) * 8);
+    float4 wc1 = *(const float4*)(ex + (size_t)(i + 2) * 8 + 4);
+    float4 wd0 = *(const float4*)(ex + (size_t)(i + 3) * 8);
+    float4 wd1 = *(const float4*)(ex + (size_t)(i + 3) * 8 + 4);
 #pragma unroll
     for (int ch = 0; ch < 4; ch++) {
       float va = bf2f(u0.us[ch]), vb = bf2f(u1.us[ch]);
-      acc[ch][0] += wa0.x * va + wb0.x * vb;
-      acc[ch][1] += wa0.y * va + wb0.y * vb;
-      acc[ch][2] += wa0.z * va + wb0.z * vb;
-      acc[ch][3] += wa0.w * va + wb0.w * vb;
-      acc[ch][4] += wa1.x * va + wb1.x * vb;
-      acc[ch][5] += wa1.y * va + wb1.y * vb;
-      acc[ch][6] += wa1.z * va + wb1.z * vb;
-      acc[ch][7] += wa1.w * va + wb1.w * vb;
+      float vc = bf2f(u2.us[ch]), vd = bf2f(u3.us[ch]);
+      acc[ch][0] += wa0.x * va + wb0.x * vb + wc0.x * vc + wd0.x * vd;
+      acc[ch][1] += wa0.y * va + wb0.y * vb + wc0.y * vc + wd0.y * vd;
+      acc[ch][2] += wa0.z * va + wb0.z * vb + wc0.z * vc + wd0.z * vd;
+      acc[ch][3] += wa0.w * va + wb0.w * vb + wc0.w * vc + wd0.w * vd;
+      acc[ch][4] += wa1.x * va + wb1.x * vb + wc1.x * vc + wd1.x * vd;
+      acc[ch][5] += wa1.y * va + wb1.y * vb + wc1.y * vc + wd1.y * vd;
+      acc[ch][6] += wa1.z * va + wb1.z * vb + wc1.z * vc + wd1.z * vd;
+      acc[ch][7] += wa1.w * va + wb1.w * vb + wc1.w * vc + wd1.w * vd;
     }
   }
   for (; i < end; i++) {
@@ -812,21 +867,24 @@
       wtin, wtpair, wtt2, wtg2, wtc1, wtg3s, apj);
 
   scan_k<<<1, 1024, 0, stream>>>(deg, rp, M);
-  fill_k<<<(E + M + 255) / 256, 256, 0, stream>>>(ei, rp, fillc, colA, E, M);
 
   int eg = (M + 3) / 4;
   int mg = (M + 63) / 64;
-
-  mgemm64_k<2, 0><<<dim3(4, mg), 256, 0, stream>>>(xb, wtin, b_in, actA, HID, M, HID, 256,
-                                                   nullptr, nullptr, nullptr, nullptr);
+  int gB = 4 * mg;
+  int fB = (E + M + 255) / 256;
+
+  fusedA_k<<<gB + fB, 256, 0, stream>>>(xb, wtin, b_in, actA, ei, rp, fillc, colA, M, E, gB);
   mgemm_dual_k<<<dim3(4, mg), 256, 0, stream>>>(actA, wtpair, b_t1, actB, hW1, M,
                                                 a_src1, a_dst1, as_, ad_);
-  mgemm64_k<0, 0><<<dim3(4, mg), 256, 0, stream>>>(actB, wtt2, b_t2, comb + HID, 2 * HID,
-                                                   M, HID, 256, nullptr, nullptr, nullptr, nullptr);
-
-  aggf_k<<<eg, 256, 0, stream>>>(rp, colA, hW1, as_, ad_, b_g1, actB, M);
-
-  mgemm64_k<0, 1><<<dim3(4, mg), 256, 0, stream>>>(actB, wtg2, nullptr, hW1, HID, M, HID, 256,
+  {
+    bf* g1buf = hW1;
+    (void)g1buf;
+  }
+  bf* g1 = hWb + (size_t)M * 1024;
+  fusedB_k<<<gB + eg, 256, 0, stream>>>(actB, wtt2, b_t2, comb + HID,
+                                        rp, colA, hW1, as_, ad_, b_g1, g1, M, gB);
+
+  mgemm64_k<0, 1><<<dim3(4, mg), 256, 0, stream>>>(g1, wtg2, nullptr, hW1, HID, M, HID, 256,
                                                    a_src2, a_dst2, as_, ad_);
   aggf_k<<<eg, 256, 0, stream>>>(rp, colA, hW1, as_, ad_, b_g2, actA, M);
 
```

New measurement: 369.6 us. 2.2% less time.
